# Optimization experiments

Measured on AMD Instinct MI355X. Metric: run time of the kernel, lower is better.

The kernel has to match this reference:

```python
import jax, jax.numpy as jnp
import numpy as np

N_HOSTS = 16
N_WINDOW = 3
GAT_IN = 3
D = 16          # d_model = gat_output_feats = n_hosts
NHEAD = 2
HD = D // NHEAD # 8
FF = 64
PROTO_DIM = 8
LATENT = N_HOSTS * D * N_WINDOW  # 768
LN_EPS = 1e-5


def _positional_encoding():
    pos = np.arange(N_WINDOW, dtype=np.float32)[:, None]
    div = np.exp(np.arange(0, D, 2, dtype=np.float32) * (-np.log(10000.0) / D))
    pe = np.zeros((N_WINDOW, D), dtype=np.float32)
    pe[:, 0::2] = np.sin(pos * div)
    pe[:, 1::2] = np.cos(pos * div)
    return jnp.asarray(pe[:, None, :])  # (n_window, 1, d_model)


def setup_inputs() -> dict:
    key = jax.random.key(0)
    ks = iter(jax.random.split(key, 40))
    p = lambda *s: jax.random.normal(next(ks), s, dtype=jnp.float32) * 0.05
    inp = {
        't': jax.random.normal(next(ks), (N_WINDOW * N_HOSTS * GAT_IN,), dtype=jnp.float32),
        's': jax.random.normal(next(ks), (N_HOSTS, PROTO_DIM), dtype=jnp.float32),
        # GAT (single head, fully connected 16-node graph)
        'gat_W': p(GAT_IN, D), 'gat_a_src': p(D), 'gat_a_dst': p(D),
        # time encoder Linear(16,16)
        'te_W': p(D, D), 'te_b': p(D),
        'pe': _positional_encoding(),
        # 2 transformer encoder layers, stacked on leading axis
        'qkv_W': p(2, 3 * D, D), 'qkv_b': p(2, 3 * D),
        'out_W': p(2, D, D), 'out_b': p(2, D),
        'ln1_g': jnp.ones((2, D), jnp.float32), 'ln1_b': jnp.zeros((2, D), jnp.float32),
        'ff1_W': p(2, FF, D), 'ff1_b': p(2, FF),
        'ff2_W': p(2, D, FF), 'ff2_b': p(2, D),
        'ln2_g': jnp.ones((2, D), jnp.float32), 'ln2_b': jnp.zeros((2, D), jnp.float32),
        # decoder heads
        'an_W': p(2 * N_HOSTS, LATENT), 'an_b': p(2 * N_HOSTS),
        'pr_W': p(PROTO_DIM * N_HOSTS, LATENT), 'pr_b': p(PROTO_DIM * N_HOSTS),
    }
    return inp


def _layer_norm(x, g, b):
    m = x.mean(-1, keepdims=True)
    v = ((x - m) ** 2).mean(-1, keepdims=True)
    return (x - m) * jax.lax.rsqrt(v + LN_EPS) * g + b


def reference(t, s, gat_W, gat_a_src, gat_a_dst, te_W, te_b, pe,
              qkv_W, qkv_b, out_W, out_b, ln1_g, ln1_b,
              ff1_W, ff1_b, ff2_W, ff2_b, ln2_g, ln2_b,
              an_W, an_b, pr_W, pr_b):
    # --- GAT over fully connected 16-host graph, per window ---
    x = t.reshape(N_WINDOW, N_HOSTS, GAT_IN)
    h = x @ gat_W                                   # (w, n, D)
    e_src = h @ gat_a_src                           # (w, n)
    e_dst = h @ gat_a_dst                           # (w, n)
    e = jax.nn.leaky_relu(e_src[:, :, None] + e_dst[:, None, :], 0.2)  # (w, src, dst)
    alpha = jax.nn.softmax(e, axis=1)               # softmax over sources, per dst
    gat_out = jax.nn.elu(jnp.einsum('wsd,wsf->wdf', alpha, h))         # (w, n, D)
    # --- time encode + positional encode (dropout = identity in eval) ---
    xe = gat_out @ te_W.T + te_b + pe               # (seq=3, batch=16, D)
    # --- 2 post-norm TransformerEncoderLayers ---
    inv_sqrt_hd = 1.0 / np.sqrt(HD).astype(np.float32)
    for l in range(2):
        qkv = xe @ qkv_W[l].T + qkv_b[l]            # (s, b, 3D)
        q, k, v = jnp.split(qkv, 3, axis=-1)
        hd = lambda z: z.reshape(N_WINDOW, N_HOSTS, NHEAD, HD).transpose(1, 2, 0, 3)  # (b,h,s,hd)
        q, k, v = hd(q), hd(k), hd(v)
        att = jax.nn.softmax(jnp.einsum('bhqd,bhkd->bhqk', q, k) * inv_sqrt_hd, axis=-1)
        ctx = jnp.einsum('bhqk,bhkd->bhqd', att, v).transpose(2, 0, 1, 3).reshape(N_WINDOW, N_HOSTS, D)
        xe = _layer_norm(xe + ctx @ out_W[l].T + out_b[l], ln1_g[l], ln1_b[l])
        ff = jax.nn.relu(xe @ ff1_W[l].T + ff1_b[l]) @ ff2_W[l].T + ff2_b[l]
        xe = _layer_norm(xe + ff, ln2_g[l], ln2_b[l])
    # --- flatten to latent (batch-major, matching permute(1,0,2).reshape) ---
    latent = xe.transpose(1, 0, 2).reshape(1, LATENT)
    # nn.LeakyReLU(True): negative_slope=True==1.0, i.e. identity (faithful to source)
    anomaly = jax.nn.leaky_relu(latent @ an_W.T + an_b, 1.0).reshape(N_HOSTS, 2)
    proto = jax.nn.sigmoid(latent @ pr_W.T + pr_b).reshape(N_HOSTS, PROTO_DIM)
    return anomaly, proto
```

## Files before the change

### kernel.cpp

```cpp
#include <hip/hip_runtime.h>
#include <hip/hip_bf16.h>


#define NW 3
#define NHOST 16
#define DM 16
#define FFD 64
#define LAT 768

typedef __hip_bfloat16 bf16;
typedef __attribute__((ext_vector_type(8))) unsigned short ushort8v;
typedef __attribute__((ext_vector_type(4))) unsigned short ushort4v;

static __device__ __forceinline__ float u2f(unsigned short u) {
    return __uint_as_float(((unsigned)u) << 16);
}

static __device__ __forceinline__ float lwf(const unsigned short* smW, int i) { return u2f(smW[i]); }
static __device__ __forceinline__ float lwf(const float* smW, int i) { return smW[i]; }

static __device__ __forceinline__ float gld(const bf16* p, int i) { return __bfloat162float(p[i]); }
static __device__ __forceinline__ float gld(const float* p, int i) { return p[i]; }
static __device__ __forceinline__ void gst(bf16* p, int i, float v) { p[i] = __float2bfloat16(v); }
static __device__ __forceinline__ void gst(float* p, int i, float v) { p[i] = v; }

static __device__ __forceinline__ void ld8g(const bf16* p, float* o) {
    ushort8v v = *(const ushort8v*)p;
    #pragma unroll
    for (int u = 0; u < 8; ++u) o[u] = u2f(v[u]);
}
static __device__ __forceinline__ void ld8g(const float* p, float* o) {
    float4 a = ((const float4*)p)[0], b = ((const float4*)p)[1];
    o[0]=a.x; o[1]=a.y; o[2]=a.z; o[3]=a.w; o[4]=b.x; o[5]=b.y; o[6]=b.z; o[7]=b.w;
}
static __device__ __forceinline__ void ld4g(const bf16* p, float* o) {
    ushort4v v = *(const ushort4v*)p;
    #pragma unroll
    for (int u = 0; u < 4; ++u) o[u] = u2f(v[u]);
}
static __device__ __forceinline__ void ld4g(const float* p, float* o) {
    float4 a = *(const float4*)p;
    o[0]=a.x; o[1]=a.y; o[2]=a.z; o[3]=a.w;
}

enum {
    OFF_T    = 0,
    OFF_GATW = 144,
    OFF_ASRC = 192,
    OFF_ADST = 208,
    OFF_TEW  = 224,
    OFF_TEB  = 480,
    OFF_PE   = 496,
    OFF_QKVW = 544,
    OFF_QKVB = 2080,
    OFF_OUTW = 2176,
    OFF_OUTB = 2688,
    OFF_LN1G = 2720,
    OFF_LN1B = 2752,
    OFF_FF1W = 2784,
    OFF_FF1B = 4832,
    OFF_FF2W = 4960,
    OFF_FF2B = 7008,
    OFF_LN2G = 7040,
    OFF_LN2B = 7072,
    TOTAL_W  = 7104
};

struct Smem {
    float h[NW][NHOST][DM];
    float esrc[NW][NHOST];
    float edst[NW][NHOST];
    float alpha[NW][NHOST][NHOST];
    float xe[NW][NHOST][DM];
    float qkv[NW][NHOST][48];
    float ctx[NW][NHOST][DM];
    float tmp[NW][NHOST][DM];
    float ffh[NW][NHOST][FFD];
};

template<typename T, typename WT>
__device__ void encode_impl(Smem& sm, WT* smW, int tid,
    const T* tin, const T* gatW, const T* asrc, const T* adst,
    const T* teW, const T* teb, const T* pe_,
    const T* qkvW, const T* qkvb, const T* outW, const T* outb,
    const T* ln1g, const T* ln1b,
    const T* ff1W, const T* ff1b, const T* ff2W, const T* ff2b,
    const T* ln2g, const T* ln2b,
    float* latent_out)
{
    constexpr int EPC = 16 / (int)sizeof(T);
    constexpr int NCHUNK = TOTAL_W / EPC;
    for (int g = tid; g < NCHUNK; g += 256) {
        int e = g * EPC;
        const T* p; int base;
        if      (e < OFF_GATW) { p = tin;   base = OFF_T; }
        else if (e < OFF_ASRC) { p = gatW;  base = OFF_GATW; }
        else if (e < OFF_ADST) { p = asrc;  base = OFF_ASRC; }
        else if (e < OFF_TEW)  { p = adst;  base = OFF_ADST; }
        else if (e < OFF_TEB)  { p = teW;   base = OFF_TEW; }
        else if (e < OFF_PE)   { p = teb;   base = OFF_TEB; }
        else if (e < OFF_QKVW) { p = pe_;   base = OFF_PE; }
        else if (e < OFF_QKVB) { p = qkvW;  base = OFF_QKVW; }
        else if (e < OFF_OUTW) { p = qkvb;  base = OFF_QKVB; }
        else if (e < OFF_OUTB) { p = outW;  base = OFF_OUTW; }
        else if (e < OFF_LN1G) { p = outb;  base = OFF_OUTB; }
        else if (e < OFF_LN1B) { p = ln1g;  base = OFF_LN1G; }
        else if (e < OFF_FF1W) { p = ln1b;  base = OFF_LN1B; }
        else if (e < OFF_FF1B) { p = ff1W;  base = OFF_FF1W; }
        else if (e < OFF_FF2W) { p = ff1b;  base = OFF_FF1B; }
        else if (e < OFF_FF2B) { p = ff2W;  base = OFF_FF2W; }
        else if (e < OFF_LN2G) { p = ff2b;  base = OFF_FF2B; }
        else if (e < OFF_LN2B) { p = ln2g;  base = OFF_LN2G; }
        else                   { p = ln2b;  base = OFF_LN2B; }
        *(ushort8v*)((unsigned char*)smW + (size_t)e * sizeof(T)) =
            *(const ushort8v*)(p + (e - base));
    }
    __syncthreads();

    for (int idx = tid; idx < NW * NHOST * DM; idx += 256) {
        int w = idx >> 8, r = idx & 255, n = r >> 4, f = r & 15;
        float acc = 0.f;
        #pragma unroll
        for (int i = 0; i < 3; ++i)
            acc += lwf(smW, OFF_T + (w * NHOST + n) * 3 + i) * lwf(smW, OFF_GATW + i * DM + f);
        sm.h[w][n][f] = acc;
    }
    __syncthreads();

    if (tid < 96) {
        int w = tid / 32, r = tid % 32, n = r & 15, which = r >> 4;
        int abase = which ? OFF_ADST : OFF_ASRC;
        float acc = 0.f;
        #pragma unroll
        for (int f = 0; f < DM; ++f) acc += sm.h[w][n][f] * lwf(smW, abase + f);
        if (which) sm.edst[w][n] = acc; else sm.esrc[w][n] = acc;
    }
    __syncthreads();

    if (tid < 48) {
        int w = tid / 16, d = tid & 15;
        float ed = sm.edst[w][d];
        float e[16];
        float mx = -1e30f;
        #pragma unroll
        for (int s = 0; s < 16; ++s) {
            float x = sm.esrc[w][s] + ed;
            x = x > 0.f ? x : 0.2f * x;
            e[s] = x;
            mx = fmaxf(mx, x);
        }
        float sum = 0.f;
        #pragma unroll
        for (int s = 0; s < 16; ++s) { e[s] = __expf(e[s] - mx); sum += e[s]; }
        float inv = 1.f / sum;
        #pragma unroll
        for (int s = 0; s < 16; ++s) sm.alpha[w][s][d] = e[s] * inv;
    }
    __syncthreads();

    for (int idx = tid; idx < NW * NHOST * DM; idx += 256) {
        int w = idx >> 8, r = idx & 255, d = r >> 4, f = r & 15;
        float acc = 0.f;
        #pragma unroll
        for (int s = 0; s < 16; ++s) acc += sm.alpha[w][s][d] * sm.h[w][s][f];
        sm.tmp[w][d][f] = acc > 0.f ? acc : (__expf(acc) - 1.f);
    }
    __syncthreads();

    for (int idx = tid; idx < NW * NHOST * DM; idx += 256) {
        int w = idx >> 8, r = idx & 255, n = r >> 4, f = r & 15;
        float acc = lwf(smW, OFF_TEB + f) + lwf(smW, OFF_PE + w * DM + f);
        #pragma unroll
        for (int g = 0; g < DM; ++g)
            acc += sm.tmp[w][n][g] * lwf(smW, OFF_TEW + f * DM + g);
        sm.xe[w][n][f] = acc;
    }
    __syncthreads();

    for (int l = 0; l < 2; ++l) {
        int qW = OFF_QKVW + l * 768, qb = OFF_QKVB + l * 48;
        for (int idx = tid; idx < NW * NHOST * 48; idx += 256) {
            int w = idx / (NHOST * 48), r = idx % (NHOST * 48), n = r / 48, j = r % 48;
            float acc = lwf(smW, qb + j);
            #pragma unroll
            for (int f = 0; f < DM; ++f) acc += sm.xe[w][n][f] * lwf(smW, qW + j * DM + f);
            sm.qkv[w][n][j] = acc;
        }
        __syncthreads();

        if (tid < 96) {
            int b = tid / 6, r = tid % 6, hh = r / 3, qs = r % 3;
            const float inv_sqrt_hd = 0.35355339059327373f;
            float sc[3];
            #pragma unroll
            for (int ks = 0; ks < 3; ++ks) {
                float acc = 0.f;
                #pragma unroll
                for (int d0 = 0; d0 < 8; ++d0)
                    acc += sm.qkv[qs][b][hh * 8 + d0] * sm.qkv[ks][b][16 + hh * 8 + d0];
                sc[ks] = acc * inv_sqrt_hd;
            }
            float mx = fmaxf(sc[0], fmaxf(sc[1], sc[2]));
            float s0 = __expf(sc[0] - mx), s1 = __expf(sc[1] - mx), s2 = __expf(sc[2] - mx);
            float inv = 1.f / (s0 + s1 + s2);
            s0 *= inv; s1 *= inv; s2 *= inv;
            #pragma unroll
            for (int d0 = 0; d0 < 8; ++d0)
                sm.ctx[qs][b][hh * 8 + d0] = s0 * sm.qkv[0][b][32 + hh * 8 + d0]
                                           + s1 * sm.qkv[1][b][32 + hh * 8 + d0]
                                           + s2 * sm.qkv[2][b][32 + hh * 8 + d0];
        }
        __syncthreads();

        int oW = OFF_OUTW + l * 256, ob = OFF_OUTB + l * 16;
        for (int idx = tid; idx < NW * NHOST * DM; idx += 256) {
            int w = idx >> 8, r = idx & 255, n = r >> 4, f = r & 15;
            float acc = lwf(smW, ob + f) + sm.xe[w][n][f];
            #pragma unroll
            for (int g = 0; g < DM; ++g) acc += sm.ctx[w][n][g] * lwf(smW, oW + f * DM + g);
            sm.tmp[w][n][f] = acc;
        }
        __syncthreads();

        if (tid < 48) {
            int w = tid / 16, n = tid & 15;
            float m = 0.f;
            #pragma unroll
            for (int f = 0; f < DM; ++f) m += sm.tmp[w][n][f];
            m *= (1.f / 16.f);
            float v = 0.f;
            #pragma unroll
            for (int f = 0; f < DM; ++f) { float d0 = sm.tmp[w][n][f] - m; v += d0 * d0; }
            v *= (1.f / 16.f);
            float rr = rsqrtf(v + 1e-5f);
            #pragma unroll
            for (int f = 0; f < DM; ++f)
                sm.xe[w][n][f] = (sm.tmp[w][n][f] - m) * rr * lwf(smW, OFF_LN1G + l * DM + f)
                               + lwf(smW, OFF_LN1B + l * DM + f);
        }
        __syncthreads();

        int f1W = OFF_FF1W + l * 1024, f1b = OFF_FF1B + l * 64;
        for (int idx = tid; idx < NW * NHOST * FFD; idx += 256) {
            int w = idx / (NHOST * FFD), r = idx % (NHOST * FFD), n = r / FFD, j = r % FFD;
            float acc = lwf(smW, f1b + j);
            #pragma unroll
            for (int f = 0; f < DM; ++f) acc += sm.xe[w][n][f] * lwf(smW, f1W + j * DM + f);
            sm.ffh[w][n][j] = fmaxf(acc, 0.f);
        }
        __syncthreads();

        int f2W = OFF_FF2W + l * 1024, f2b = OFF_FF2B + l * 16;
        for (int idx = tid; idx < NW * NHOST * DM; idx += 256) {
            int w = idx >> 8, r = idx & 255, n = r >> 4, f = r & 15;
            float acc = lwf(smW, f2b + f) + sm.xe[w][n][f];
            #pragma unroll
            for (int j = 0; j < FFD; ++j) acc += sm.ffh[w][n][j] * lwf(smW, f2W + f * FFD + j);
            sm.tmp[w][n][f] = acc;
        }
        __syncthreads();

        if (tid < 48) {
            int w = tid / 16, n = tid & 15;
            float m = 0.f;
            #pragma unroll
            for (int f = 0; f < DM; ++f) m += sm.tmp[w][n][f];
            m *= (1.f / 16.f);
            float v = 0.f;
            #pragma unroll
            for (int f = 0; f < DM; ++f) { float d0 = sm.tmp[w][n][f] - m; v += d0 * d0; }
            v *= (1.f / 16.f);
            float rr = rsqrtf(v + 1e-5f);
            #pragma unroll
            for (int f = 0; f < DM; ++f)
                sm.xe[w][n][f] = (sm.tmp[w][n][f] - m) * rr * lwf(smW, OFF_LN2G + l * DM + f)
                               + lwf(smW, OFF_LN2B + l * DM + f);
        }
        __syncthreads();
    }

    for (int idx = tid; idx < LAT; idx += 256) {
        int w = idx >> 8, r = idx & 255, n = r >> 4, f = r & 15;
        latent_out[n * 48 + w * DM + f] = sm.xe[w][n][f];
    }
}

__global__ void __launch_bounds__(256) txf_encode(
    const void* t, const void* gat_W, const void* a_src, const void* a_dst,
    const void* te_W, const void* te_b, const void* pe,
    const void* qkv_W, const void* qkv_b, const void* out_W, const void* out_b,
    const void* ln1_g, const void* ln1_b,
    const void* ff1_W, const void* ff1_b, const void* ff2_W, const void* ff2_b,
    const void* ln2_g, const void* ln2_b,
    float* latent_out)
{
    __shared__ Smem sm;
    __shared__ __align__(16) unsigned char wbuf[TOTAL_W * 4];
    const int tid = threadIdx.x;
    unsigned w0 = *(const unsigned*)ln1_g;
    if (w0 == 0x3F803F80u) {
        encode_impl<bf16, unsigned short>(sm, (unsigned short*)wbuf, tid,
            (const bf16*)t, (const bf16*)gat_W, (const bf16*)a_src, (const bf16*)a_dst,
            (const bf16*)te_W, (const bf16*)te_b, (const bf16*)pe,
            (const bf16*)qkv_W, (const bf16*)qkv_b, (const bf16*)out_W, (const bf16*)out_b,
            (const bf16*)ln1_g, (const bf16*)ln1_b,
            (const bf16*)ff1_W, (const bf16*)ff1_b, (const bf16*)ff2_W, (const bf16*)ff2_b,
            (const bf16*)ln2_g, (const bf16*)ln2_b, latent_out);
    } else {
        encode_impl<float, float>(sm, (float*)wbuf, tid,
            (const float*)t, (const float*)gat_W, (const float*)a_src, (const float*)a_dst,
            (const float*)te_W, (const float*)te_b, (const float*)pe,
            (const float*)qkv_W, (const float*)qkv_b, (const float*)out_W, (const float*)out_b,
            (const float*)ln1_g, (const float*)ln1_b,
            (const float*)ff1_W, (const float*)ff1_b, (const float*)ff2_W, (const float*)ff2_b,
            (const float*)ln2_g, (const float*)ln2_b, latent_out);
    }
}

template<typename T>
__device__ void decode_impl(const T* an_W, const T* an_b, const T* pr_W, const T* pr_b,
                            const float* latent, T* out)
{
    const int o = blockIdx.x;
    const int l = threadIdx.x;
    const T* Wr = (o < 32) ? (an_W + o * LAT) : (pr_W + (o - 32) * LAT);

    float wv8[8], wv4[4];
    ld8g(Wr + l * 8, wv8);
    ld4g(Wr + 512 + l * 4, wv4);
    float4 a = ((const float4*)latent)[2 * l];
    float4 b = ((const float4*)latent)[2 * l + 1];
    float4 c = ((const float4*)(latent + 512))[l];

    float acc = wv8[0]*a.x + wv8[1]*a.y + wv8[2]*a.z + wv8[3]*a.w
              + wv8[4]*b.x + wv8[5]*b.y + wv8[6]*b.z + wv8[7]*b.w
              + wv4[0]*c.x + wv4[1]*c.y + wv4[2]*c.z + wv4[3]*c.w;

    #pragma unroll
    for (int m = 1; m < 64; m <<= 1) acc += __shfl_xor(acc, m);

    if (l == 0) {
        if (o < 32) {
            gst(out, o, acc + gld(an_b, o));
        } else {
            float z = acc + gld(pr_b, o - 32);
            gst(out, o, 1.f / (1.f + __expf(-z)));
        }
    }
}

__global__ void __launch_bounds__(64) txf_decode(
    const void* an_W, const void* an_b, const void* pr_W, const void* pr_b,
    const void* ln1_g, const float* latent, void* out)
{
    unsigned w0 = *(const unsigned*)ln1_g;
    if (w0 == 0x3F803F80u) {
        decode_impl<bf16>((const bf16*)an_W, (const bf16*)an_b,
                          (const bf16*)pr_W, (const bf16*)pr_b, latent, (bf16*)out);
    } else {
        decode_impl<float>((const float*)an_W, (const float*)an_b,
                           (const float*)pr_W, (const float*)pr_b, latent, (float*)out);
    }
}

extern "C" void kernel_launch(void* const* d_in, const int* in_sizes, int n_in,
                              void* d_out, int out_size, void* d_ws, size_t ws_size,
                              hipStream_t stream) {
    float* latent = (float*)d_ws;

    txf_encode<<<1, 256, 0, stream>>>(
        d_in[0],
        d_in[2], d_in[3], d_in[4],
        d_in[5], d_in[6], d_in[7],
        d_in[8], d_in[9], d_in[10], d_in[11],
        d_in[12], d_in[13],
        d_in[14], d_in[15], d_in[16], d_in[17],
        d_in[18], d_in[19],
        latent);

    txf_decode<<<160, 64, 0, stream>>>(
        d_in[20], d_in[21], d_in[22], d_in[23],
        d_in[12],
        latent, d_out);
}
```

Before: 123.5 us.

## Fuse encoder and decoder into one kernel with redundant per-block encoding

Replaces the two-kernel pipeline (single-block encoder writing latent to workspace, then a 160-block decoder) with one 160-block kernel. Every block recomputes the full encoder in shared memory, then computes one output row from its prefetched weight row. The goal is to remove the second launch and the global round-trip for the latent. The cost is 160x redundant encoder compute and weight loads, plus a cross-wave reduction through shared memory.

```diff
diff --git a/kernel.cpp b/kernel.cpp
--- a/kernel.cpp
+++ b/kernel.cpp
@@ -10,38 +10,18 @@
 
 typedef __hip_bfloat16 bf16;
 typedef __attribute__((ext_vector_type(8))) unsigned short ushort8v;
-typedef __attribute__((ext_vector_type(4))) unsigned short ushort4v;
 
 static __device__ __forceinline__ float u2f(unsigned short u) {
     return __uint_as_float(((unsigned)u) << 16);
 }
 
-static __device__ __forceinline__ float lwf(const unsigned short* smW, int i) { return u2f(smW[i]); }
-static __device__ __forceinline__ float lwf(const float* smW, int i) { return smW[i]; }
+static __device__ __forceinline__ float lwf(const unsigned short* a, int i) { return u2f(a[i]); }
+static __device__ __forceinline__ float lwf(const float* a, int i) { return a[i]; }
 
 static __device__ __forceinline__ float gld(const bf16* p, int i) { return __bfloat162float(p[i]); }
 static __device__ __forceinline__ float gld(const float* p, int i) { return p[i]; }
 static __device__ __forceinline__ void gst(bf16* p, int i, float v) { p[i] = __float2bfloat16(v); }
 static __device__ __forceinline__ void gst(float* p, int i, float v) { p[i] = v; }
-
-static __device__ __forceinline__ void ld8g(const bf16* p, float* o) {
-    ushort8v v = *(const ushort8v*)p;
-    #pragma unroll
-    for (int u = 0; u < 8; ++u) o[u] = u2f(v[u]);
-}
-static __device__ __forceinline__ void ld8g(const float* p, float* o) {
-    float4 a = ((const float4*)p)[0], b = ((const float4*)p)[1];
-    o[0]=a.x; o[1]=a.y; o[2]=a.z; o[3]=a.w; o[4]=b.x; o[5]=b.y; o[6]=b.z; o[7]=b.w;
-}
-static __device__ __forceinline__ void ld4g(const bf16* p, float* o) {
-    ushort4v v = *(const ushort4v*)p;
-    #pragma unroll
-    for (int u = 0; u < 4; ++u) o[u] = u2f(v[u]);
-}
-static __device__ __forceinline__ void ld4g(const float* p, float* o) {
-    float4 a = *(const float4*)p;
-    o[0]=a.x; o[1]=a.y; o[2]=a.z; o[3]=a.w;
-}
 
 enum {
     OFF_T    = 0,
@@ -76,44 +56,56 @@
     float ctx[NW][NHOST][DM];
     float tmp[NW][NHOST][DM];
     float ffh[NW][NHOST][FFD];
+    float latent[LAT];
+    float part[4];
 };
 
 template<typename T, typename WT>
-__device__ void encode_impl(Smem& sm, WT* smW, int tid,
-    const T* tin, const T* gatW, const T* asrc, const T* adst,
-    const T* teW, const T* teb, const T* pe_,
-    const T* qkvW, const T* qkvb, const T* outW, const T* outb,
-    const T* ln1g, const T* ln1b,
-    const T* ff1W, const T* ff1b, const T* ff2W, const T* ff2b,
-    const T* ln2g, const T* ln2b,
-    float* latent_out)
+__device__ void run_all(Smem& sm, WT* smW, int tid, int o,
+    const T* t, const T* gat_W, const T* a_src, const T* a_dst,
+    const T* te_W, const T* te_b, const T* pe,
+    const T* qkv_W, const T* qkv_b, const T* out_W, const T* out_b,
+    const T* ln1_g, const T* ln1_b,
+    const T* ff1_W, const T* ff1_b, const T* ff2_W, const T* ff2_b,
+    const T* ln2_g, const T* ln2_b,
+    const T* an_W, const T* an_b, const T* pr_W, const T* pr_b,
+    T* out)
 {
-    constexpr int EPC = 16 / (int)sizeof(T);
-    constexpr int NCHUNK = TOTAL_W / EPC;
-    for (int g = tid; g < NCHUNK; g += 256) {
-        int e = g * EPC;
-        const T* p; int base;
-        if      (e < OFF_GATW) { p = tin;   base = OFF_T; }
-        else if (e < OFF_ASRC) { p = gatW;  base = OFF_GATW; }
-        else if (e < OFF_ADST) { p = asrc;  base = OFF_ASRC; }
-        else if (e < OFF_TEW)  { p = adst;  base = OFF_ADST; }
-        else if (e < OFF_TEB)  { p = teW;   base = OFF_TEW; }
-        else if (e < OFF_PE)   { p = teb;   base = OFF_TEB; }
-        else if (e < OFF_QKVW) { p = pe_;   base = OFF_PE; }
-        else if (e < OFF_QKVB) { p = qkvW;  base = OFF_QKVW; }
-        else if (e < OFF_OUTW) { p = qkvb;  base = OFF_QKVB; }
-        else if (e < OFF_OUTB) { p = outW;  base = OFF_OUTW; }
-        else if (e < OFF_LN1G) { p = outb;  base = OFF_OUTB; }
-        else if (e < OFF_LN1B) { p = ln1g;  base = OFF_LN1G; }
-        else if (e < OFF_FF1W) { p = ln1b;  base = OFF_LN1B; }
-        else if (e < OFF_FF1B) { p = ff1W;  base = OFF_FF1W; }
-        else if (e < OFF_FF2W) { p = ff1b;  base = OFF_FF1B; }
-        else if (e < OFF_FF2B) { p = ff2W;  base = OFF_FF2W; }
-        else if (e < OFF_LN2G) { p = ff2b;  base = OFF_FF2B; }
-        else if (e < OFF_LN2B) { p = ln2g;  base = OFF_LN2G; }
-        else                   { p = ln2b;  base = OFF_LN2B; }
-        *(ushort8v*)((unsigned char*)smW + (size_t)e * sizeof(T)) =
-            *(const ushort8v*)(p + (e - base));
+    T wr0{}, wr1{}, wr2{}, wr3{};
+    if (tid < 192) {
+        const T* Wr = (o < 32) ? (an_W + o * LAT) : (pr_W + (o - 32) * LAT);
+        wr0 = Wr[tid * 4];     wr1 = Wr[tid * 4 + 1];
+        wr2 = Wr[tid * 4 + 2]; wr3 = Wr[tid * 4 + 3];
+    }
+
+    {
+        constexpr int EPC = 16 / (int)sizeof(T);
+        constexpr int NCHUNK = TOTAL_W / EPC;
+        for (int g = tid; g < NCHUNK; g += 256) {
+            int e = g * EPC;
+            const T* p; int base;
+            if      (e < OFF_GATW) { p = t;      base = OFF_T; }
+            else if (e < OFF_ASRC) { p = gat_W;  base = OFF_GATW; }
+            else if (e < OFF_ADST) { p = a_src;  base = OFF_ASRC; }
+            else if (e < OFF_TEW)  { p = a_dst;  base = OFF_ADST; }
+            else if (e < OFF_TEB)  { p = te_W;   base = OFF_TEW; }
+            else if (e < OFF_PE)   { p = te_b;   base = OFF_TEB; }
+            else if (e < OFF_QKVW) { p = pe;     base = OFF_PE; }
+            else if (e < OFF_QKVB) { p = qkv_W;  base = OFF_QKVW; }
+            else if (e < OFF_OUTW) { p = qkv_b;  base = OFF_QKVB; }
+            else if (e < OFF_OUTB) { p = out_W;  base = OFF_OUTW; }
+            else if (e < OFF_LN1G) { p = out_b;  base = OFF_OUTB; }
+            else if (e < OFF_LN1B) { p = ln1_g;  base = OFF_LN1G; }
+            else if (e < OFF_FF1W) { p = ln1_b;  base = OFF_LN1B; }
+            else if (e < OFF_FF1B) { p = ff1_W;  base = OFF_FF1W; }
+            else if (e < OFF_FF2W) { p = ff1_b;  base = OFF_FF1B; }
+            else if (e < OFF_FF2B) { p = ff2_W;  base = OFF_FF2W; }
+            else if (e < OFF_LN2G) { p = ff2_b;  base = OFF_FF2B; }
+            else if (e < OFF_LN2B) { p = ln2_g;  base = OFF_LN2G; }
+            else                   { p = ln2_b;  base = OFF_LN2B; }
+            *(ushort8v*)((unsigned char*)smW + (size_t)e * sizeof(T)) =
+                *(const ushort8v*)(p + (e - base));
+        }
     }
     __syncthreads();
 
@@ -177,6 +169,7 @@
     }
     __syncthreads();
 
+    #pragma unroll 1
     for (int l = 0; l < 2; ++l) {
         int qW = OFF_QKVW + l * 768, qb = OFF_QKVB + l * 48;
         for (int idx = tid; idx < NW * NHOST * 48; idx += 256) {
@@ -281,94 +274,75 @@
 
     for (int idx = tid; idx < LAT; idx += 256) {
         int w = idx >> 8, r = idx & 255, n = r >> 4, f = r & 15;
-        latent_out[n * 48 + w * DM + f] = sm.xe[w][n][f];
+        sm.latent[n * 48 + w * DM + f] = sm.xe[w][n][f];
+    }
+    __syncthreads();
+
+    float acc = 0.f;
+    if (tid < 192) {
+        int e0 = tid * 4;
+        acc = sm.latent[e0]     * gld(&wr0, 0)
+            + sm.latent[e0 + 1] * gld(&wr1, 0)
+            + sm.latent[e0 + 2] * gld(&wr2, 0)
+            + sm.latent[e0 + 3] * gld(&wr3, 0);
+    }
+    #pragma unroll
+    for (int m = 1; m < 64; m <<= 1) acc += __shfl_xor(acc, m);
+    if ((tid & 63) == 0) sm.part[tid >> 6] = acc;
+    __syncthreads();
+    if (tid == 0) {
+        float s = sm.part[0] + sm.part[1] + sm.part[2] + sm.part[3];
+        if (o < 32) {
+            gst(out, o, s + gld(an_b, o));
+        } else {
+            float z = s + gld(pr_b, o - 32);
+            gst(out, o, 1.f / (1.f + __expf(-z)));
+        }
     }
 }
 
-__global__ void __launch_bounds__(256) txf_encode(
+__global__ void __launch_bounds__(256) txf_fused(
     const void* t, const void* gat_W, const void* a_src, const void* a_dst,
     const void* te_W, const void* te_b, const void* pe,
     const void* qkv_W, const void* qkv_b, const void* out_W, const void* out_b,
     const void* ln1_g, const void* ln1_b,
     const void* ff1_W, const void* ff1_b, const void* ff2_W, const void* ff2_b,
     const void* ln2_g, const void* ln2_b,
-    float* latent_out)
+    const void* an_W, const void* an_b, const void* pr_W, const void* pr_b,
+    void* out)
 {
     __shared__ Smem sm;
     __shared__ __align__(16) unsigned char wbuf[TOTAL_W * 4];
     const int tid = threadIdx.x;
+    const int o = blockIdx.x;
     unsigned w0 = *(const unsigned*)ln1_g;
     if (w0 == 0x3F803F80u) {
-        encode_impl<bf16, unsigned short>(sm, (unsigned short*)wbuf, tid,
+        run_all<bf16, unsigned short>(sm, (unsigned short*)wbuf, tid, o,
             (const bf16*)t, (const bf16*)gat_W, (const bf16*)a_src, (const bf16*)a_dst,
             (const bf16*)te_W, (const bf16*)te_b, (const bf16*)pe,
             (const bf16*)qkv_W, (const bf16*)qkv_b, (const bf16*)out_W, (const bf16*)out_b,
             (const bf16*)ln1_g, (const bf16*)ln1_b,
             (const bf16*)ff1_W, (const bf16*)ff1_b, (const bf16*)ff2_W, (const bf16*)ff2_b,
-            (const bf16*)ln2_g, (const bf16*)ln2_b, latent_out);
+            (const bf16*)ln2_g, (const bf16*)ln2_b,
+            (const bf16*)an_W, (const bf16*)an_b, (const bf16*)pr_W, (const bf16*)pr_b,
+            (bf16*)out);
     } else {
-        encode_impl<float, float>(sm, (float*)wbuf, tid,
+        run_all<float, float>(sm, (float*)wbuf, tid, o,
             (const float*)t, (const float*)gat_W, (const float*)a_src, (const float*)a_dst,
             (const float*)te_W, (const float*)te_b, (const float*)pe,
             (const float*)qkv_W, (const float*)qkv_b, (const float*)out_W, (const float*)out_b,
             (const float*)ln1_g, (const float*)ln1_b,
             (const float*)ff1_W, (const float*)ff1_b, (const float*)ff2_W, (const float*)ff2_b,
-            (const float*)ln2_g, (const float*)ln2_b, latent_out);
-    }
-}
-
-template<typename T>
-__device__ void decode_impl(const T* an_W, const T* an_b, const T* pr_W, const T* pr_b,
-                            const float* latent, T* out)
-{
-    const int o = blockIdx.x;
-    const int l = threadIdx.x;
-    const T* Wr = (o < 32) ? (an_W + o * LAT) : (pr_W + (o - 32) * LAT);
-
-    float wv8[8], wv4[4];
-    ld8g(Wr + l * 8, wv8);
-    ld4g(Wr + 512 + l * 4, wv4);
-    float4 a = ((const float4*)latent)[2 * l];
-    float4 b = ((const float4*)latent)[2 * l + 1];
-    float4 c = ((const float4*)(latent + 512))[l];
-
-    float acc = wv8[0]*a.x + wv8[1]*a.y + wv8[2]*a.z + wv8[3]*a.w
-              + wv8[4]*b.x + wv8[5]*b.y + wv8[6]*b.z + wv8[7]*b.w
-              + wv4[0]*c.x + wv4[1]*c.y + wv4[2]*c.z + wv4[3]*c.w;
-
-    #pragma unroll
-    for (int m = 1; m < 64; m <<= 1) acc += __shfl_xor(acc, m);
-
-    if (l == 0) {
-        if (o < 32) {
-            gst(out, o, acc + gld(an_b, o));
-        } else {
-            float z = acc + gld(pr_b, o - 32);
-            gst(out, o, 1.f / (1.f + __expf(-z)));
-        }
-    }
-}
-
-__global__ void __launch_bounds__(64) txf_decode(
-    const void* an_W, const void* an_b, const void* pr_W, const void* pr_b,
-    const void* ln1_g, const float* latent, void* out)
-{
-    unsigned w0 = *(const unsigned*)ln1_g;
-    if (w0 == 0x3F803F80u) {
-        decode_impl<bf16>((const bf16*)an_W, (const bf16*)an_b,
-                          (const bf16*)pr_W, (const bf16*)pr_b, latent, (bf16*)out);
-    } else {
-        decode_impl<float>((const float*)an_W, (const float*)an_b,
-                           (const float*)pr_W, (const float*)pr_b, latent, (float*)out);
+            (const float*)ln2_g, (const float*)ln2_b,
+            (const float*)an_W, (const float*)an_b, (const float*)pr_W, (const float*)pr_b,
+            (float*)out);
     }
 }
 
 extern "C" void kernel_launch(void* const* d_in, const int* in_sizes, int n_in,
                               void* d_out, int out_size, void* d_ws, size_t ws_size,
                               hipStream_t stream) {
-    float* latent = (float*)d_ws;
-
-    txf_encode<<<1, 256, 0, stream>>>(
+    txf_fused<<<160, 256, 0, stream>>>(
         d_in[0],
         d_in[2], d_in[3], d_in[4],
         d_in[5], d_in[6], d_in[7],
@@ -376,10 +350,6 @@
         d_in[12], d_in[13],
         d_in[14], d_in[15], d_in[16], d_in[17],
         d_in[18], d_in[19],
-        latent);
-
-    txf_decode<<<160, 64, 0, stream>>>(
         d_in[20], d_in[21], d_in[22], d_in[23],
-        d_in[12],
-        latent, d_out);
+        d_out);
 }
```

Result: slower. 127.0 us (+2.9%).
